# Performance work log

Hardware: AMD Instinct MI355X
Metric: run time of the kernel (lower is better)

Reference implementation:

```python
import jax, jax.numpy as jnp
import numpy as np

B, L, S, H, E = 4, 1024, 1024, 8, 64
MASK_SCALE = 10000.0
TAU_MIN, TAU_MAX = 0.1, 5.0
TH_MIN, TH_MAX = 0.01, 0.99
EPS = 1e-8


def setup_inputs() -> dict:
    k0 = jax.random.key(0)
    ks = jax.random.split(k0, 5)
    query = jax.random.normal(ks[0], (B, L, H, E), jnp.float32)
    key = jax.random.normal(ks[1], (B, S, H, E), jnp.float32)
    value = jax.random.normal(ks[2], (B, S, H, E), jnp.float32)
    # positions: monotone per batch -> standard causal mask
    pos = jnp.arange(B * L, dtype=jnp.float32).reshape(B, L, 1)
    phi = jax.random.normal(ks[3], (H, L, S), jnp.float32)
    # uniform noise for Gumbel-sigmoid reparameterization (torch.rand_like)
    u = jax.random.uniform(ks[4], (H, L, S), jnp.float32)
    log_tau = jnp.asarray(np.log(2.0), jnp.float32)
    threshold = jnp.asarray(0.5, jnp.float32)
    return {"query": query, "key": key, "value": value, "pos": pos,
            "phi": phi, "u": u, "log_tau": log_tau, "threshold": threshold,
            "causal_mask": 1}


def reference(query, key, value, pos, phi, u, log_tau, threshold, causal_mask):
    Bq, Lq, Hq, Eq = query.shape
    scale = 1.0 / np.sqrt(Eq).astype(np.float32)
    # raw attention scores (B,H,L,S)
    scores = jnp.einsum('blhe,bshe->bhls', query, key)
    if causal_mask:
        p = pos[..., 0]                       # (B,L)
        # M[b,i,j] = -inf where p[b,j] > p[b,i]
        neg_inf = jnp.asarray(-jnp.inf, scores.dtype)
        M = jnp.where(p[:, None, :] > p[:, :, None], neg_inf, 0.0)  # (B,L,S)
        scores = scores + M[:, None, :, :]
    # learnable DAG mask via Gumbel-sigmoid relaxation
    tau = jnp.clip(jnp.exp(log_tau), TAU_MIN, TAU_MAX)
    gumbel = jnp.log(u + EPS) - jnp.log(1.0 - u + EPS)
    m_relaxed = jax.nn.sigmoid((gumbel + phi) / tau)      # (H,L,S)
    thresh = jnp.clip(threshold, TH_MIN, TH_MAX)
    phi_mask = -MASK_SCALE * jax.nn.relu(thresh - m_relaxed)
    scores = scores + phi_mask[None]                      # broadcast over batch
    att = jax.nn.softmax(scale * scores, axis=-1)          # (B,H,L,S)
    # per-query attention entropy (B,H,L)
    entropy = -jnp.sum(att * jnp.log(jnp.clip(att, EPS, None)), axis=-1)
    entropy = jnp.nan_to_num(entropy, nan=0.0)
    # dropout p=0 (eval) -> A = att
    V = jnp.einsum('bhls,bshd->blhd', att, value)          # (B,L,H,E)
    return V, att, entropy
```

## Files before the change

### kernel.cpp

```cpp
#include <hip/hip_runtime.h>

#define BN 4
#define LN 1024
#define SN 1024
#define HN 8
#define EN 64
#define OFF_ATT (BN * LN * HN * EN)
#define OFF_ENT (OFF_ATT + BN * HN * LN * SN)

#define WS_MW 0u
#define WS_KB 16777216u
#define WS_VT (WS_KB + 4194304u)

#define APITCH 2064

#define LOG2E 1.44269504f
#define LN2 0.69314718f
#define SCL (0.125f * LOG2E)

typedef __attribute__((ext_vector_type(8))) __bf16 bf16x8;
typedef __attribute__((ext_vector_type(4))) float f32x4;
typedef __attribute__((ext_vector_type(4))) unsigned int uint4v;
typedef __attribute__((ext_vector_type(2))) unsigned int uint2v;
typedef __attribute__((ext_vector_type(4))) _Float16 f16x4;

__device__ __forceinline__ void decode_block(int x, int& b, int& lb) {
  int lbLo = x & 7;
  b = (x >> 3) & 3;
  lb = (x >> 5) * 8 + lbLo;
}

__device__ __forceinline__ unsigned int rne2(float x, float y) {
  unsigned int ux = __float_as_uint(x), uy = __float_as_uint(y);
  ux += 0x7fffu + ((ux >> 16) & 1u);
  uy += 0x7fffu + ((uy >> 16) & 1u);
  return (ux >> 16) | (uy & 0xffff0000u);
}

__device__ __forceinline__ uint4v pack8_rne(float4 a, float4 b) {
  return uint4v{rne2(a.x, a.y), rne2(a.z, a.w), rne2(b.x, b.y), rne2(b.z, b.w)};
}

__global__ __launch_bounds__(256) void k_prep(
    const float* __restrict__ kk, const float* __restrict__ vv,
    const float* __restrict__ phi, const float* __restrict__ u,
    const float* __restrict__ p_logtau, const float* __restrict__ p_thresh,
    _Float16* __restrict__ mw, unsigned short* __restrict__ kb,
    unsigned short* __restrict__ vT) {
  const int bx = blockIdx.x;
  if (bx < 8192) {
    const float tau = fminf(fmaxf(__expf(p_logtau[0]), 0.1f), 5.0f);
    const float rtau = 1.0f / tau;
    const float thr = fminf(fmaxf(p_thresh[0], 0.01f), 0.99f);
    int idx = (bx * 256 + threadIdx.x) * 4;
    float4 u4 = *(const float4*)(u + idx);
    float4 p4 = *(const float4*)(phi + idx);
    float uu[4] = {u4.x, u4.y, u4.z, u4.w};
    float pp[4] = {p4.x, p4.y, p4.z, p4.w};
    f16x4 o;
#pragma unroll
    for (int i = 0; i < 4; ++i) {
      float g = __logf(__fdividef(uu[i] + 1e-8f, 1.0f - uu[i] + 1e-8f));
      float z = (g + pp[i]) * rtau;
      float sig = __fdividef(1.0f, 1.0f + __expf(-z));
      o[i] = (_Float16)(-10000.0f * fmaxf(thr - sig, 0.0f) * SCL);
    }
    *(f16x4*)(mw + idx) = o;
  } else if (bx < 9216) {
    int gid = (bx - 8192) * 256 + threadIdx.x;
    int e8 = gid & 7;
    int tmp = gid >> 3;
    int h = tmp & 7;
    int bs = tmp >> 3;
    int s = bs & 1023;
    int b = bs >> 10;
    const float* src = kk + (size_t)gid * 8;
    float4 a = *(const float4*)src;
    float4 bq = *(const float4*)(src + 4);
    *(uint4v*)(kb + (((size_t)(b * 8 + h) * 1024 + s) * 64) + e8 * 8) =
        pack8_rne(a, bq);
  } else {
    int gid = (bx - 9216) * 256 + threadIdx.x;
    int s8 = gid & 127;
    int t1 = gid >> 7;
    int e = t1 & 63;
    int t2 = t1 >> 6;
    int h = t2 & 7;
    int b = t2 >> 3;
    float x[8];
#pragma unroll
    for (int j = 0; j < 8; ++j)
      x[j] = vv[((size_t)(b * 1024 + s8 * 8 + j) * 8 + h) * 64 + e];
    uint4v pv = pack8_rne(float4{x[0], x[1], x[2], x[3]},
                          float4{x[4], x[5], x[6], x[7]});
    *(uint4v*)(vT + ((size_t)(b * 8 + h) * 64 + e) * 1024 + s8 * 8) = pv;
  }
}

__global__ __launch_bounds__(512, 4) void k_fused(
    const float* __restrict__ q, const unsigned short* __restrict__ kb,
    const unsigned short* __restrict__ vT, const _Float16* __restrict__ mw,
    const int* __restrict__ p_causal, float* __restrict__ out) {
  int b, lb;
  decode_block(blockIdx.x, b, lb);
  const int h = blockIdx.y;
  const int tid = threadIdx.x;
  const int w = __builtin_amdgcn_readfirstlane(tid >> 6);
  const int c = tid & 63;
  const int cl = c & 15;
  const int cg = c >> 4;

  __shared__ __align__(16) unsigned char lds_att[32 * APITCH];
  __shared__ float redM[2][8][16], redZ[2][8][16], redE[2][8][16];

  const int causal = p_causal[0];
  const unsigned short* kbb = kb + ((size_t)(b * 8 + h) * 1024) * 64;

  {
    const unsigned char* gmask =
        (const unsigned char*)(mw + ((size_t)h * LN + lb * 32) * SN);
    uint4v mk[8];
#pragma unroll
    for (int i = 0; i < 8; ++i)
      mk[i] = *(const uint4v*)(gmask + i * 8192 + tid * 16);
#pragma unroll
    for (int i = 0; i < 8; ++i) {
      int goff = i * 8192 + tid * 16;
      *(uint4v*)(lds_att + (goff >> 11) * APITCH + (goff & 2047)) = mk[i];
    }
  }

  uint4v qf[2][2];
#pragma unroll
  for (int qt = 0; qt < 2; ++qt)
#pragma unroll
    for (int cc = 0; cc < 2; ++cc) {
      const float* qp = q + (((size_t)b * LN + lb * 32 + qt * 16 + cl) * HN + h) * EN +
                        cc * 32 + cg * 8;
      float4 a = *(const float4*)qp;
      float4 bq = *(const float4*)(qp + 4);
      qf[qt][cc] = pack8_rne(a, bq);
    }

  f32x4 accs[16];
#pragma unroll
  for (int tgb = 0; tgb < 2; ++tgb) {
    uint4v kf[4][2];
#pragma unroll
    for (int t2 = 0; t2 < 4; ++t2)
#pragma unroll
      for (int cc = 0; cc < 2; ++cc)
        kf[t2][cc] = *(const uint4v*)(kbb +
                                      (size_t)(w * 128 + (tgb * 4 + t2) * 16 + cl) * 64 +
                                      cc * 32 + cg * 8);
#pragma unroll
    for (int t2 = 0; t2 < 4; ++t2)
#pragma unroll
      for (int qt = 0; qt < 2; ++qt) {
        f32x4 acc = f32x4{0.f, 0.f, 0.f, 0.f};
#pragma unroll
        for (int cc = 0; cc < 2; ++cc)
          acc = __builtin_amdgcn_mfma_f32_16x16x32_bf16(
              __builtin_bit_cast(bf16x8, kf[t2][cc]),
              __builtin_bit_cast(bf16x8, qf[qt][cc]), acc, 0, 0, 0);
        accs[qt * 8 + tgb * 4 + t2] = acc;
      }
  }

  __syncthreads();

  float mx[2];
#pragma unroll
  for (int qt = 0; qt < 2; ++qt) {
    const int l = lb * 32 + qt * 16 + cl;
    const unsigned char* mrow = lds_att + (qt * 16 + cl) * APITCH;
    float m = -3.0e38f;
#pragma unroll
    for (int tg = 0; tg < 8; ++tg) {
      const int s0 = w * 128 + tg * 16 + cg * 4;
      f16x4 m4 = *(const f16x4*)(mrow + s0 * 2);
#pragma unroll
      for (int r = 0; r < 4; ++r) {
        float v = fmaf(accs[qt * 8 + tg][r], SCL, (float)m4[r]);
        bool maskd = (causal != 0) && (s0 + r > l);
        v = maskd ? -1.0e30f : v;
        accs[qt * 8 + tg][r] = v;
        m = fmaxf(m, v);
      }
    }
    m = fmaxf(m, __shfl_xor(m, 16, 64));
    m = fmaxf(m, __shfl_xor(m, 32, 64));
    mx[qt] = m;

    float z = 0.f, e = 0.f;
#pragma unroll
    for (int tg = 0; tg < 8; ++tg) {
#pragma unroll
      for (int r = 0; r < 4; ++r) {
        float tt = accs[qt * 8 + tg][r] - m;
        float ex = exp2f(tt);
        z += ex;
        e = fmaf(ex, tt, e);
        accs[qt * 8 + tg][r] = ex;
      }
    }
    z += __shfl_xor(z, 16, 64);
    z += __shfl_xor(z, 32, 64);
    e += __shfl_xor(e, 16, 64);
    e += __shfl_xor(e, 32, 64);
    if (cg == 0) { redM[qt][w][cl] = m; redZ[qt][w][cl] = z; redE[qt][w][cl] = e; }
  }
  __syncthreads();

#pragma unroll
  for (int qt = 0; qt < 2; ++qt) {
    const int l = lb * 32 + qt * 16 + cl;
    float M = redM[qt][0][cl];
#pragma unroll
    for (int i = 1; i < 8; ++i) M = fmaxf(M, redM[qt][i][cl]);
    float Z = 0.f, E = 0.f;
#pragma unroll
    for (int i = 0; i < 8; ++i) {
      float dm = redM[qt][i][cl] - M;
      float sci = exp2f(dm);
      Z += sci * redZ[qt][i][cl];
      E = fmaf(sci, fmaf(dm, redZ[qt][i][cl], redE[qt][i][cl]), E);
    }
    const float rz = __fdividef(1.0f, Z);
    if (w == 0 && cg == 0)
      out[OFF_ENT + ((size_t)b * HN + h) * LN + l] = LN2 * (__log2f(Z) - E * rz);

    const float scw = exp2f(mx[qt] - M) * rz;
    unsigned char* arow = lds_att + (qt * 16 + cl) * APITCH;
#pragma unroll
    for (int tg = 0; tg < 8; ++tg) {
      const int s0 = w * 128 + tg * 16 + cg * 4;
      float ax = accs[qt * 8 + tg][0] * scw, ay = accs[qt * 8 + tg][1] * scw;
      float az = accs[qt * 8 + tg][2] * scw, aw = accs[qt * 8 + tg][3] * scw;
      uint2v pk = uint2v{rne2(ax, ay), rne2(az, aw)};
      *(uint2v*)(arow + s0 * 2) = pk;
    }
  }

  const int et = w & 3, sh = w >> 2;
  const unsigned short* vbb =
      vT + ((size_t)(b * 8 + h) * 64 + et * 16 + cl) * 1024 + sh * 512;
  uint4v vf0[8];
#pragma unroll
  for (int j = 0; j < 8; ++j)
    vf0[j] = *(const uint4v*)(vbb + j * 32 + cg * 8);

  __syncthreads();

  f32x4 acc00 = f32x4{0.f, 0.f, 0.f, 0.f}, acc01 = f32x4{0.f, 0.f, 0.f, 0.f};
  f32x4 acc10 = f32x4{0.f, 0.f, 0.f, 0.f}, acc11 = f32x4{0.f, 0.f, 0.f, 0.f};
#pragma unroll
  for (int scb = 0; scb < 2; ++scb) {
    uint4v vf[8];
    if (scb == 0) {
#pragma unroll
      for (int j = 0; j < 8; ++j) vf[j] = vf0[j];
    } else {
#pragma unroll
      for (int j = 0; j < 8; ++j)
        vf[j] = *(const uint4v*)(vbb + 256 + j * 32 + cg * 8);
    }
#pragma unroll
    for (int qt = 0; qt < 2; ++qt) {
      uint4v af[8];
#pragma unroll
      for (int j = 0; j < 8; ++j)
        af[j] = *(const uint4v*)(lds_att + (qt * 16 + cl) * APITCH +
                                 (sh * 512 + scb * 256 + j * 32 + cg * 8) * 2);
#pragma unroll
      for (int j = 0; j < 8; ++j) {
        bf16x8 a8 = __builtin_bit_cast(bf16x8, vf[j]);
        bf16x8 b8 = __builtin_bit_cast(bf16x8, af[j]);
        if (qt == 0) {
          if (j & 1)
            acc01 = __builtin_amdgcn_mfma_f32_16x16x32_bf16(a8, b8, acc01, 0, 0, 0);
          else
            acc00 = __builtin_amdgcn_mfma_f32_16x16x32_bf16(a8, b8, acc00, 0, 0, 0);
        } else {
          if (j & 1)
            acc11 = __builtin_amdgcn_mfma_f32_16x16x32_bf16(a8, b8, acc11, 0, 0, 0);
          else
            acc10 = __builtin_amdgcn_mfma_f32_16x16x32_bf16(a8, b8, acc10, 0, 0, 0);
        }
      }
    }
  }
  f32x4 sum0 = acc00 + acc01;
  f32x4 sum1 = acc10 + acc11;

  {
    float* abase = out + OFF_ATT + (((size_t)b * HN + h) * LN + lb * 32) * SN;
#pragma unroll
    for (int rr = 0; rr < 4; ++rr) {
      const int row = w * 4 + rr;
      const unsigned char* src = lds_att + row * APITCH;
      float* dst = abase + (size_t)row * SN;
#pragma unroll
      for (int it = 0; it < 4; ++it) {
        uint2v pk = *(const uint2v*)(src + it * 512 + c * 8);
        f32x4 o = f32x4{__uint_as_float(pk.x << 16),
                        __uint_as_float(pk.x & 0xffff0000u),
                        __uint_as_float(pk.y << 16),
                        __uint_as_float(pk.y & 0xffff0000u)};
        __builtin_nontemporal_store(o, (f32x4*)(dst + it * 256 + c * 4));
      }
    }
  }

  __syncthreads();

  *(f32x4*)(lds_att + cl * APITCH + sh * 1024 + (et * 16 + cg * 4) * 4) = sum0;
  *(f32x4*)(lds_att + (16 + cl) * APITCH + sh * 1024 + (et * 16 + cg * 4) * 4) = sum1;

  __syncthreads();

  {
    const int r = tid >> 4, e4 = tid & 15;
    f32x4 p0 = *(const f32x4*)(lds_att + r * APITCH + e4 * 16);
    f32x4 p1 = *(const f32x4*)(lds_att + r * APITCH + 1024 + e4 * 16);
    f32x4 s = p0 + p1;
    float* dst = out + (((size_t)b * LN + lb * 32 + r) * HN + h) * EN + e4 * 4;
    __builtin_nontemporal_store(s, (f32x4*)dst);
  }
}

extern "C" void kernel_launch(void* const* d_in, const int* in_sizes, int n_in,
                              void* d_out, int out_size, void* d_ws, size_t ws_size,
                              hipStream_t stream) {
  (void)in_sizes; (void)n_in; (void)out_size; (void)ws_size;
  const float* q   = (const float*)d_in[0];
  const float* k   = (const float*)d_in[1];
  const float* v   = (const float*)d_in[2];
  const float* phi = (const float*)d_in[4];
  const float* u   = (const float*)d_in[5];
  const float* lt  = (const float*)d_in[6];
  const float* th  = (const float*)d_in[7];
  const int*   cm  = (const int*)d_in[8];
  float* out = (float*)d_out;

  _Float16* mw = (_Float16*)((char*)d_ws + WS_MW);
  unsigned short* kb = (unsigned short*)((char*)d_ws + WS_KB);
  unsigned short* vT = (unsigned short*)((char*)d_ws + WS_VT);

  k_prep<<<dim3(10240), dim3(256), 0, stream>>>(k, v, phi, u, lt, th, mw, kb, vT);
  k_fused<<<dim3(128, 8, 1), dim3(512), 0, stream>>>(q, kb, vT, mw, cm, out);
}
```

Before: 93.18 us.

## Fuse Gumbel mask computation into attention kernel and loop over batch per block

```diff
diff --git a/kernel.cpp b/kernel.cpp
--- a/kernel.cpp
+++ b/kernel.cpp
@@ -8,9 +8,8 @@
 #define OFF_ATT (BN * LN * HN * EN)
 #define OFF_ENT (OFF_ATT + BN * HN * LN * SN)
 
-#define WS_MW 0u
-#define WS_KB 16777216u
-#define WS_VT (WS_KB + 4194304u)
+#define WS_KB 0u
+#define WS_VT 4194304u
 
 #define APITCH 2064
 
@@ -24,12 +23,6 @@
 typedef __attribute__((ext_vector_type(2))) unsigned int uint2v;
 typedef __attribute__((ext_vector_type(4))) _Float16 f16x4;
 
-__device__ __forceinline__ void decode_block(int x, int& b, int& lb) {
-  int lbLo = x & 7;
-  b = (x >> 3) & 3;
-  lb = (x >> 5) * 8 + lbLo;
-}
-
 __device__ __forceinline__ unsigned int rne2(float x, float y) {
   unsigned int ux = __float_as_uint(x), uy = __float_as_uint(y);
   ux += 0x7fffu + ((ux >> 16) & 1u);
@@ -43,31 +36,10 @@
 
 __global__ __launch_bounds__(256) void k_prep(
     const float* __restrict__ kk, const float* __restrict__ vv,
-    const float* __restrict__ phi, const float* __restrict__ u,
-    const float* __restrict__ p_logtau, const float* __restrict__ p_thresh,
-    _Float16* __restrict__ mw, unsigned short* __restrict__ kb,
-    unsigned short* __restrict__ vT) {
+    unsigned short* __restrict__ kb, unsigned short* __restrict__ vT) {
   const int bx = blockIdx.x;
-  if (bx < 8192) {
-    const float tau = fminf(fmaxf(__expf(p_logtau[0]), 0.1f), 5.0f);
-    const float rtau = 1.0f / tau;
-    const float thr = fminf(fmaxf(p_thresh[0], 0.01f), 0.99f);
-    int idx = (bx * 256 + threadIdx.x) * 4;
-    float4 u4 = *(const float4*)(u + idx);
-    float4 p4 = *(const float4*)(phi + idx);
-    float uu[4] = {u4.x, u4.y, u4.z, u4.w};
-    float pp[4] = {p4.x, p4.y, p4.z, p4.w};
-    f16x4 o;
-#pragma unroll
-    for (int i = 0; i < 4; ++i) {
-      float g = __logf(__fdividef(uu[i] + 1e-8f, 1.0f - uu[i] + 1e-8f));
-      float z = (g + pp[i]) * rtau;
-      float sig = __fdividef(1.0f, 1.0f + __expf(-z));
-      o[i] = (_Float16)(-10000.0f * fmaxf(thr - sig, 0.0f) * SCL);
-    }
-    *(f16x4*)(mw + idx) = o;
-  } else if (bx < 9216) {
-    int gid = (bx - 8192) * 256 + threadIdx.x;
+  if (bx < 1024) {
+    int gid = bx * 256 + threadIdx.x;
     int e8 = gid & 7;
     int tmp = gid >> 3;
     int h = tmp & 7;
@@ -80,7 +52,7 @@
     *(uint4v*)(kb + (((size_t)(b * 8 + h) * 1024 + s) * 64) + e8 * 8) =
         pack8_rne(a, bq);
   } else {
-    int gid = (bx - 9216) * 256 + threadIdx.x;
+    int gid = (bx - 1024) * 256 + threadIdx.x;
     int s8 = gid & 127;
     int t1 = gid >> 7;
     int e = t1 & 63;
@@ -97,235 +69,256 @@
   }
 }
 
-__global__ __launch_bounds__(512, 4) void k_fused(
+__global__ __launch_bounds__(1024, 4) void k_fused(
     const float* __restrict__ q, const unsigned short* __restrict__ kb,
-    const unsigned short* __restrict__ vT, const _Float16* __restrict__ mw,
-    const int* __restrict__ p_causal, float* __restrict__ out) {
-  int b, lb;
-  decode_block(blockIdx.x, b, lb);
-  const int h = blockIdx.y;
+    const unsigned short* __restrict__ vT, const float* __restrict__ phi,
+    const float* __restrict__ uarr, const float* __restrict__ p_logtau,
+    const float* __restrict__ p_thresh, const int* __restrict__ p_causal,
+    float* __restrict__ out) {
+  const int h = blockIdx.x;
+  const int lb = blockIdx.y;
   const int tid = threadIdx.x;
   const int w = __builtin_amdgcn_readfirstlane(tid >> 6);
   const int c = tid & 63;
   const int cl = c & 15;
   const int cg = c >> 4;
 
+  __shared__ __align__(16) unsigned char lds_mask[32 * APITCH];
   __shared__ __align__(16) unsigned char lds_att[32 * APITCH];
-  __shared__ float redM[2][8][16], redZ[2][8][16], redE[2][8][16];
+  __shared__ float redM[2][16][16], redZ[2][16][16], redE[2][16][16];
 
   const int causal = p_causal[0];
-  const unsigned short* kbb = kb + ((size_t)(b * 8 + h) * 1024) * 64;
+  const float tau = fminf(fmaxf(__expf(p_logtau[0]), 0.1f), 5.0f);
+  const float rtau = 1.0f / tau;
+  const float thr = fminf(fmaxf(p_thresh[0], 0.01f), 0.99f);
 
   {
-    const unsigned char* gmask =
-        (const unsigned char*)(mw + ((size_t)h * LN + lb * 32) * SN);
-    uint4v mk[8];
-#pragma unroll
-    for (int i = 0; i < 8; ++i)
-      mk[i] = *(const uint4v*)(gmask + i * 8192 + tid * 16);
+    const size_t base = ((size_t)h * LN + lb * 32) * SN;
+    const float* phb = phi + base;
+    const float* ub = uarr + base;
 #pragma unroll
     for (int i = 0; i < 8; ++i) {
-      int goff = i * 8192 + tid * 16;
-      *(uint4v*)(lds_att + (goff >> 11) * APITCH + (goff & 2047)) = mk[i];
+      int elem = i * 4096 + tid * 4;
+      float4 p4 = *(const float4*)(phb + elem);
+      float4 u4 = *(const float4*)(ub + elem);
+      float pp[4] = {p4.x, p4.y, p4.z, p4.w};
+      float uu[4] = {u4.x, u4.y, u4.z, u4.w};
+      f16x4 o;
+#pragma unroll
+      for (int j = 0; j < 4; ++j) {
+        float g = __logf(__fdividef(uu[j] + 1e-8f, 1.0f - uu[j] + 1e-8f));
+        float z = (g + pp[j]) * rtau;
+        float sig = __fdividef(1.0f, 1.0f + __expf(-z));
+        o[j] = (_Float16)(-10000.0f * fmaxf(thr - sig, 0.0f) * SCL);
+      }
+      int row = elem >> 10;
+      *(f16x4*)(lds_mask + row * APITCH + (elem & 1023) * 2) = o;
     }
   }
 
-  uint4v qf[2][2];
-#pragma unroll
-  for (int qt = 0; qt < 2; ++qt)
-#pragma unroll
-    for (int cc = 0; cc < 2; ++cc) {
-      const float* qp = q + (((size_t)b * LN + lb * 32 + qt * 16 + cl) * HN + h) * EN +
-                        cc * 32 + cg * 8;
-      float4 a = *(const float4*)qp;
-      float4 bq = *(const float4*)(qp + 4);
-      qf[qt][cc] = pack8_rne(a, bq);
-    }
-
-  f32x4 accs[16];
-#pragma unroll
-  for (int tgb = 0; tgb < 2; ++tgb) {
-    uint4v kf[4][2];
-#pragma unroll
-    for (int t2 = 0; t2 < 4; ++t2)
-#pragma unroll
-      for (int cc = 0; cc < 2; ++cc)
-        kf[t2][cc] = *(const uint4v*)(kbb +
-                                      (size_t)(w * 128 + (tgb * 4 + t2) * 16 + cl) * 64 +
-                                      cc * 32 + cg * 8);
-#pragma unroll
-    for (int t2 = 0; t2 < 4; ++t2)
+  const int et = w & 3, sq = w >> 2;
+
+  for (int b = 0; b < BN; ++b) {
+    const unsigned short* kbb = kb + ((size_t)(b * 8 + h) * 1024) * 64;
+
+    uint4v qf[2][2];
+#pragma unroll
+    for (int qt = 0; qt < 2; ++qt)
+#pragma unroll
+      for (int cc = 0; cc < 2; ++cc) {
+        const float* qp = q +
+            (((size_t)b * LN + lb * 32 + qt * 16 + cl) * HN + h) * EN +
+            cc * 32 + cg * 8;
+        float4 a = *(const float4*)qp;
+        float4 bq = *(const float4*)(qp + 4);
+        qf[qt][cc] = pack8_rne(a, bq);
+      }
+
+    f32x4 accs[8];
+#pragma unroll
+    for (int tgb = 0; tgb < 2; ++tgb) {
+      uint4v kf[2][2];
+#pragma unroll
+      for (int t2 = 0; t2 < 2; ++t2)
+#pragma unroll
+        for (int cc = 0; cc < 2; ++cc)
+          kf[t2][cc] = *(const uint4v*)(kbb +
+              (size_t)(w * 64 + (tgb * 2 + t2) * 16 + cl) * 64 +
+              cc * 32 + cg * 8);
+#pragma unroll
+      for (int t2 = 0; t2 < 2; ++t2)
+#pragma unroll
+        for (int qt = 0; qt < 2; ++qt) {
+          f32x4 acc = f32x4{0.f, 0.f, 0.f, 0.f};
+#pragma unroll
+          for (int cc = 0; cc < 2; ++cc)
+            acc = __builtin_amdgcn_mfma_f32_16x16x32_bf16(
+                __builtin_bit_cast(bf16x8, kf[t2][cc]),
+                __builtin_bit_cast(bf16x8, qf[qt][cc]), acc, 0, 0, 0);
+          accs[qt * 4 + tgb * 2 + t2] = acc;
+        }
+    }
+
+    __syncthreads();
+
+    float mx[2];
+#pragma unroll
+    for (int qt = 0; qt < 2; ++qt) {
+      const int l = lb * 32 + qt * 16 + cl;
+      const unsigned char* mrow = lds_mask + (qt * 16 + cl) * APITCH;
+      float m = -3.0e38f;
+#pragma unroll
+      for (int tg = 0; tg < 4; ++tg) {
+        const int s0 = w * 64 + tg * 16 + cg * 4;
+        f16x4 m4 = *(const f16x4*)(mrow + s0 * 2);
+#pragma unroll
+        for (int r = 0; r < 4; ++r) {
+          float v = fmaf(accs[qt * 4 + tg][r], SCL, (float)m4[r]);
+          bool maskd = (causal != 0) && (s0 + r > l);
+          v = maskd ? -1.0e30f : v;
+          accs[qt * 4 + tg][r] = v;
+          m = fmaxf(m, v);
+        }
+      }
+      m = fmaxf(m, __shfl_xor(m, 16, 64));
+      m = fmaxf(m, __shfl_xor(m, 32, 64));
+      mx[qt] = m;
+
+      float z = 0.f, e = 0.f;
+#pragma unroll
+      for (int tg = 0; tg < 4; ++tg) {
+#pragma unroll
+        for (int r = 0; r < 4; ++r) {
+          float tt = accs[qt * 4 + tg][r] - m;
+          float ex = exp2f(tt);
+          z += ex;
+          e = fmaf(ex, tt, e);
+          accs[qt * 4 + tg][r] = ex;
+        }
+      }
+      z += __shfl_xor(z, 16, 64);
+      z += __shfl_xor(z, 32, 64);
+      e += __shfl_xor(e, 16, 64);
+      e += __shfl_xor(e, 32, 64);
+      if (cg == 0) { redM[qt][w][cl] = m; redZ[qt][w][cl] = z; redE[qt][w][cl] = e; }
+    }
+    __syncthreads();
+
+#pragma unroll
+    for (int qt = 0; qt < 2; ++qt) {
+      const int l = lb * 32 + qt * 16 + cl;
+      float M = redM[qt][0][cl];
+#pragma unroll
+      for (int i = 1; i < 16; ++i) M = fmaxf(M, redM[qt][i][cl]);
+      float Z = 0.f, E = 0.f;
+#pragma unroll
+      for (int i = 0; i < 16; ++i) {
+        float dm = redM[qt][i][cl] - M;
+        float sci = exp2f(dm);
+        Z += sci * redZ[qt][i][cl];
+        E = fmaf(sci, fmaf(dm, redZ[qt][i][cl], redE[qt][i][cl]), E);
+      }
+      const float rz = __fdividef(1.0f, Z);
+      if (w == 0 && cg == 0)
+        out[OFF_ENT + ((size_t)b * HN + h) * LN + l] =
+            LN2 * (__log2f(Z) - E * rz);
+
+      const float scw = exp2f(mx[qt] - M) * rz;
+      unsigned char* arow = lds_att + (qt * 16 + cl) * APITCH;
+#pragma unroll
+      for (int tg = 0; tg < 4; ++tg) {
+        const int s0 = w * 64 + tg * 16 + cg * 4;
+        float ax = accs[qt * 4 + tg][0] * scw, ay = accs[qt * 4 + tg][1] * scw;
+        float az = accs[qt * 4 + tg][2] * scw, aw = accs[qt * 4 + tg][3] * scw;
+        *(uint2v*)(arow + s0 * 2) = uint2v{rne2(ax, ay), rne2(az, aw)};
+      }
+    }
+
+    const unsigned short* vbb =
+        vT + ((size_t)(b * 8 + h) * 64 + et * 16 + cl) * 1024 + sq * 256;
+    uint4v vf0[4];
+#pragma unroll
+    for (int j = 0; j < 4; ++j)
+      vf0[j] = *(const uint4v*)(vbb + j * 32 + cg * 8);
+
+    __syncthreads();
+
+    f32x4 acc00 = f32x4{0.f, 0.f, 0.f, 0.f}, acc01 = f32x4{0.f, 0.f, 0.f, 0.f};
+    f32x4 acc10 = f32x4{0.f, 0.f, 0.f, 0.f}, acc11 = f32x4{0.f, 0.f, 0.f, 0.f};
+#pragma unroll
+    for (int scb = 0; scb < 2; ++scb) {
+      uint4v vf[4];
+      if (scb == 0) {
+#pragma unroll
+        for (int j = 0; j < 4; ++j) vf[j] = vf0[j];
+      } else {
+#pragma unroll
+        for (int j = 0; j < 4; ++j)
+          vf[j] = *(const uint4v*)(vbb + 128 + j * 32 + cg * 8);
+      }
 #pragma unroll
       for (int qt = 0; qt < 2; ++qt) {
-        f32x4 acc = f32x4{0.f, 0.f, 0.f, 0.f};
-#pragma unroll
-        for (int cc = 0; cc < 2; ++cc)
-          acc = __builtin_amdgcn_mfma_f32_16x16x32_bf16(
-              __builtin_bit_cast(bf16x8, kf[t2][cc]),
-              __builtin_bit_cast(bf16x8, qf[qt][cc]), acc, 0, 0, 0);
-        accs[qt * 8 + tgb * 4 + t2] = acc;
-      }
-  }
-
-  __syncthreads();
-
-  float mx[2];
-#pragma unroll
-  for (int qt = 0; qt < 2; ++qt) {
-    const int l = lb * 32 + qt * 16 + cl;
-    const unsigned char* mrow = lds_att + (qt * 16 + cl) * APITCH;
-    float m = -3.0e38f;
-#pragma unroll
-    for (int tg = 0; tg < 8; ++tg) {
-      const int s0 = w * 128 + tg * 16 + cg * 4;
-      f16x4 m4 = *(const f16x4*)(mrow + s0 * 2);
-#pragma unroll
-      for (int r = 0; r < 4; ++r) {
-        float v = fmaf(accs[qt * 8 + tg][r], SCL, (float)m4[r]);
-        bool maskd = (causal != 0) && (s0 + r > l);
-        v = maskd ? -1.0e30f : v;
-        accs[qt * 8 + tg][r] = v;
-        m = fmaxf(m, v);
-      }
-    }
-    m = fmaxf(m, __shfl_xor(m, 16, 64));
-    m = fmaxf(m, __shfl_xor(m, 32, 64));
-    mx[qt] = m;
-
-    float z = 0.f, e = 0.f;
-#pragma unroll
-    for (int tg = 0; tg < 8; ++tg) {
-#pragma unroll
-      for (int r = 0; r < 4; ++r) {
-        float tt = accs[qt * 8 + tg][r] - m;
-        float ex = exp2f(tt);
-        z += ex;
-        e = fmaf(ex, tt, e);
-        accs[qt * 8 + tg][r] = ex;
-      }
-    }
-    z += __shfl_xor(z, 16, 64);
-    z += __shfl_xor(z, 32, 64);
-    e += __shfl_xor(e, 16, 64);
-    e += __shfl_xor(e, 32, 64);
-    if (cg == 0) { redM[qt][w][cl] = m; redZ[qt][w][cl] = z; redE[qt][w][cl] = e; }
-  }
-  __syncthreads();
-
-#pragma unroll
-  for (int qt = 0; qt < 2; ++qt) {
-    const int l = lb * 32 + qt * 16 + cl;
-    float M = redM[qt][0][cl];
-#pragma unroll
-    for (int i = 1; i < 8; ++i) M = fmaxf(M, redM[qt][i][cl]);
-    float Z = 0.f, E = 0.f;
-#pragma unroll
-    for (int i = 0; i < 8; ++i) {
-      float dm = redM[qt][i][cl] - M;
-      float sci = exp2f(dm);
-      Z += sci * redZ[qt][i][cl];
-      E = fmaf(sci, fmaf(dm, redZ[qt][i][cl], redE[qt][i][cl]), E);
-    }
-    const float rz = __fdividef(1.0f, Z);
-    if (w == 0 && cg == 0)
-      out[OFF_ENT + ((size_t)b * HN + h) * LN + l] = LN2 * (__log2f(Z) - E * rz);
-
-    const float scw = exp2f(mx[qt] - M) * rz;
-    unsigned char* arow = lds_att + (qt * 16 + cl) * APITCH;
-#pragma unroll
-    for (int tg = 0; tg < 8; ++tg) {
-      const int s0 = w * 128 + tg * 16 + cg * 4;
-      float ax = accs[qt * 8 + tg][0] * scw, ay = accs[qt * 8 + tg][1] * scw;
-      float az = accs[qt * 8 + tg][2] * scw, aw = accs[qt * 8 + tg][3] * scw;
-      uint2v pk = uint2v{rne2(ax, ay), rne2(az, aw)};
-      *(uint2v*)(arow + s0 * 2) = pk;
-    }
-  }
-
-  const int et = w & 3, sh = w >> 2;
-  const unsigned short* vbb =
-      vT + ((size_t)(b * 8 + h) * 64 + et * 16 + cl) * 1024 + sh * 512;
-  uint4v vf0[8];
-#pragma unroll
-  for (int j = 0; j < 8; ++j)
-    vf0[j] = *(const uint4v*)(vbb + j * 32 + cg * 8);
-
-  __syncthreads();
-
-  f32x4 acc00 = f32x4{0.f, 0.f, 0.f, 0.f}, acc01 = f32x4{0.f, 0.f, 0.f, 0.f};
-  f32x4 acc10 = f32x4{0.f, 0.f, 0.f, 0.f}, acc11 = f32x4{0.f, 0.f, 0.f, 0.f};
-#pragma unroll
-  for (int scb = 0; scb < 2; ++scb) {
-    uint4v vf[8];
-    if (scb == 0) {
-#pragma unroll
-      for (int j = 0; j < 8; ++j) vf[j] = vf0[j];
-    } else {
-#pragma unroll
-      for (int j = 0; j < 8; ++j)
-        vf[j] = *(const uint4v*)(vbb + 256 + j * 32 + cg * 8);
-    }
-#pragma unroll
-    for (int qt = 0; qt < 2; ++qt) {
-      uint4v af[8];
-#pragma unroll
-      for (int j = 0; j < 8; ++j)
-        af[j] = *(const uint4v*)(lds_att + (qt * 16 + cl) * APITCH +
-                                 (sh * 512 + scb * 256 + j * 32 + cg * 8) * 2);
-#pragma unroll
-      for (int j = 0; j < 8; ++j) {
-        bf16x8 a8 = __builtin_bit_cast(bf16x8, vf[j]);
-        bf16x8 b8 = __builtin_bit_cast(bf16x8, af[j]);
-        if (qt == 0) {
-          if (j & 1)
-            acc01 = __builtin_amdgcn_mfma_f32_16x16x32_bf16(a8, b8, acc01, 0, 0, 0);
-          else
-            acc00 = __builtin_amdgcn_mfma_f32_16x16x32_bf16(a8, b8, acc00, 0, 0, 0);
-        } else {
-          if (j & 1)
-            acc11 = __builtin_amdgcn_mfma_f32_16x16x32_bf16(a8, b8, acc11, 0, 0, 0);
-          else
-            acc10 = __builtin_amdgcn_mfma_f32_16x16x32_bf16(a8, b8, acc10, 0, 0, 0);
-        }
-      }
-    }
-  }
-  f32x4 sum0 = acc00 + acc01;
-  f32x4 sum1 = acc10 + acc11;
-
-  {
-    float* abase = out + OFF_ATT + (((size_t)b * HN + h) * LN + lb * 32) * SN;
-#pragma unroll
-    for (int rr = 0; rr < 4; ++rr) {
-      const int row = w * 4 + rr;
-      const unsigned char* src = lds_att + row * APITCH;
-      float* dst = abase + (size_t)row * SN;
-#pragma unroll
-      for (int it = 0; it < 4; ++it) {
-        uint2v pk = *(const uint2v*)(src + it * 512 + c * 8);
-        f32x4 o = f32x4{__uint_as_float(pk.x << 16),
-                        __uint_as_float(pk.x & 0xffff0000u),
-                        __uint_as_float(pk.y << 16),
-                        __uint_as_float(pk.y & 0xffff0000u)};
-        __builtin_nontemporal_store(o, (f32x4*)(dst + it * 256 + c * 4));
-      }
-    }
-  }
-
-  __syncthreads();
-
-  *(f32x4*)(lds_att + cl * APITCH + sh * 1024 + (et * 16 + cg * 4) * 4) = sum0;
-  *(f32x4*)(lds_att + (16 + cl) * APITCH + sh * 1024 + (et * 16 + cg * 4) * 4) = sum1;
-
-  __syncthreads();
-
-  {
-    const int r = tid >> 4, e4 = tid & 15;
-    f32x4 p0 = *(const f32x4*)(lds_att + r * APITCH + e4 * 16);
-    f32x4 p1 = *(const f32x4*)(lds_att + r * APITCH + 1024 + e4 * 16);
-    f32x4 s = p0 + p1;
-    float* dst = out + (((size_t)b * LN + lb * 32 + r) * HN + h) * EN + e4 * 4;
-    __builtin_nontemporal_store(s, (f32x4*)dst);
+        uint4v af[4];
+#pragma unroll
+        for (int j = 0; j < 4; ++j)
+          af[j] = *(const uint4v*)(lds_att + (qt * 16 + cl) * APITCH +
+                                   (sq * 256 + scb * 128 + j * 32 + cg * 8) * 2);
+#pragma unroll
+        for (int j = 0; j < 4; ++j) {
+          bf16x8 a8 = __builtin_bit_cast(bf16x8, vf[j]);
+          bf16x8 b8 = __builtin_bit_cast(bf16x8, af[j]);
+          if (qt == 0) {
+            if (j & 1)
+              acc01 = __builtin_amdgcn_mfma_f32_16x16x32_bf16(a8, b8, acc01, 0, 0, 0);
+            else
+              acc00 = __builtin_amdgcn_mfma_f32_16x16x32_bf16(a8, b8, acc00, 0, 0, 0);
+          } else {
+            if (j & 1)
+              acc11 = __builtin_amdgcn_mfma_f32_16x16x32_bf16(a8, b8, acc11, 0, 0, 0);
+            else
+              acc10 = __builtin_amdgcn_mfma_f32_16x16x32_bf16(a8, b8, acc10, 0, 0, 0);
+          }
+        }
+      }
+    }
+    f32x4 sum0 = acc00 + acc01;
+    f32x4 sum1 = acc10 + acc11;
+
+    {
+      float* abase = out + OFF_ATT + (((size_t)b * HN + h) * LN + lb * 32) * SN;
+#pragma unroll
+      for (int rr = 0; rr < 2; ++rr) {
+        const int row = w * 2 + rr;
+        const unsigned char* src = lds_att + row * APITCH;
+        float* dst = abase + (size_t)row * SN;
+#pragma unroll
+        for (int it = 0; it < 4; ++it) {
+          uint2v pk = *(const uint2v*)(src + it * 512 + c * 8);
+          f32x4 o = f32x4{__uint_as_float(pk.x << 16),
+                          __uint_as_float(pk.x & 0xffff0000u),
+                          __uint_as_float(pk.y << 16),
+                          __uint_as_float(pk.y & 0xffff0000u)};
+          __builtin_nontemporal_store(o, (f32x4*)(dst + it * 256 + c * 4));
+        }
+      }
+    }
+
+    __syncthreads();
+
+    *(f32x4*)(lds_att + cl * APITCH + sq * 256 + et * 64 + cg * 16) = sum0;
+    *(f32x4*)(lds_att + (16 + cl) * APITCH + sq * 256 + et * 64 + cg * 16) = sum1;
+
+    __syncthreads();
+
+    if (tid < 512) {
+      const int r = tid >> 4, e4 = tid & 15;
+      f32x4 s = f32x4{0.f, 0.f, 0.f, 0.f};
+#pragma unroll
+      for (int q_ = 0; q_ < 4; ++q_)
+        s += *(const f32x4*)(lds_att + r * APITCH + q_ * 256 + e4 * 16);
+      float* dst = out + (((size_t)b * LN + lb * 32 + r) * HN + h) * EN + e4 * 4;
+      __builtin_nontemporal_store(s, (f32x4*)dst);
+    }
   }
 }
 
@@ -343,10 +336,10 @@
   const int*   cm  = (const int*)d_in[8];
   float* out = (float*)d_out;
 
-  _Float16* mw = (_Float16*)((char*)d_ws + WS_MW);
   unsigned short* kb = (unsigned short*)((char*)d_ws + WS_KB);
   unsigned short* vT = (unsigned short*)((char*)d_ws + WS_VT);
 
-  k_prep<<<dim3(10240), dim3(256), 0, stream>>>(k, v, phi, u, lt, th, mw, kb, vT);
-  k_fused<<<dim3(128, 8, 1), dim3(512), 0, stream>>>(q, kb, vT, mw, cm, out);
-}
+  k_prep<<<dim3(2048), dim3(256), 0, stream>>>(k, v, kb, vT);
+  k_fused<<<dim3(8, 32, 1), dim3(1024), 0, stream>>>(q, kb, vT, phi, u, lt, th,
+                                                     cm, out);
+}
```

New measurement: 110.1 us. 18.2% more time.
